# Kernel optimization log

Measured on AMD Instinct MI355X. Metric: run time of the kernel, lower is better.

Reference implementation:

```python
import jax, jax.numpy as jnp
import numpy as np

N_NODES = 100000
N_EDGES = 300000
NUM_GRAPHS = 2000
IN_DIM = 82
HIDDEN = 256


def _gcn_conv(x, src, dst, dinv, W, b):
    # GCNConv: out = D^-1/2 (A + I) D^-1/2 (x W) + b
    xW = x @ W  # [N, H]
    norm = dinv[src] * dinv[dst]  # [E]
    agg = jax.ops.segment_sum(xW[src] * norm[:, None], dst, num_segments=N_NODES)
    self_loop = xW * (dinv * dinv)[:, None]
    return agg + self_loop + b


def setup_inputs() -> dict:
    key = jax.random.key(0)
    ks = jax.random.split(key, 8)
    x = jax.random.normal(ks[0], (N_NODES, IN_DIM), dtype=jnp.float32)
    edge_index = jax.random.randint(ks[1], (2, N_EDGES), 0, N_NODES, dtype=jnp.int64)
    batch = jnp.sort(jax.random.randint(ks[2], (N_NODES,), 0, NUM_GRAPHS, dtype=jnp.int64))
    W1 = jax.random.normal(ks[3], (IN_DIM, HIDDEN), dtype=jnp.float32) * (1.0 / np.sqrt(IN_DIM))
    W2 = jax.random.normal(ks[4], (HIDDEN, HIDDEN), dtype=jnp.float32) * (1.0 / np.sqrt(HIDDEN))
    W3 = jax.random.normal(ks[5], (HIDDEN, HIDDEN), dtype=jnp.float32) * (1.0 / np.sqrt(HIDDEN))
    b1 = jnp.zeros((HIDDEN,), jnp.float32)
    b2 = jnp.zeros((HIDDEN,), jnp.float32)
    b3 = jnp.zeros((HIDDEN,), jnp.float32)
    return {"x": x, "edge_index": edge_index, "batch": batch, "num_graphs": NUM_GRAPHS,
            "W1": W1, "b1": b1, "W2": W2, "b2": b2, "W3": W3, "b3": b3}


def reference(x, edge_index, batch, num_graphs, W1, b1, W2, b2, W3, b3):
    src, dst = edge_index[0], edge_index[1]
    # symmetric normalization with added self-loops (PyG gcn_norm)
    deg = jax.ops.segment_sum(jnp.ones_like(dst, dtype=x.dtype), dst, num_segments=N_NODES) + 1.0
    dinv = jax.lax.rsqrt(deg)
    h = jax.nn.relu(_gcn_conv(x, src, dst, dinv, W1, b1))
    h = jax.nn.relu(_gcn_conv(h, src, dst, dinv, W2, b2))
    h = jax.nn.relu(_gcn_conv(h, src, dst, dinv, W3, b3))
    return jax.ops.segment_max(h, batch, num_segments=num_graphs)  # [G, H]
```

## Files before the change

kernel.cpp:

```cpp
#include <hip/hip_runtime.h>
#include <cstdint>
#include <cstddef>

#define N_NODES 100000
#define N_EDGES 300000
#define N_GRAPHS 2000
#define HID 256
#define INDIM 82
#define XCPAD 84
#define K1PAD 128
#define N_TILES ((N_NODES + 255) / 256)
#define SCAN_CHUNK 2048
#define NBLK_SCAN ((N_NODES + SCAN_CHUNK - 1) / SCAN_CHUNK)

typedef __bf16 bf16x8 __attribute__((ext_vector_type(8)));
typedef float f32x4 __attribute__((ext_vector_type(4)));

__device__ __forceinline__ unsigned short f2bf(float f) {
    union { __bf16 h; unsigned short u; } v;
    v.h = (__bf16)f;
    return v.u;
}
__device__ __forceinline__ float bf2f(unsigned short s) {
    return __uint_as_float(((unsigned int)s) << 16);
}
__device__ __forceinline__ int sig(int c) { return ((c & 15) << 4) | (c >> 4); }

__global__ void k_cnt_acc(const int* __restrict__ ei, int* cnt) {
    int e = blockIdx.x * 256 + threadIdx.x;
    if (e < N_EDGES) atomicAdd(&cnt[ei[N_EDGES + e]], 1);
}

__global__ __launch_bounds__(256) void k_scan1(const int* __restrict__ cnt, int* __restrict__ off,
                                               int* __restrict__ partial) {
    __shared__ int sdata[256];
    const int base = blockIdx.x * SCAN_CHUNK;
    const int t = threadIdx.x;
    int v[8];
    int s = 0;
#pragma unroll
    for (int i = 0; i < 8; ++i) {
        int idx = base + t * 8 + i;
        v[i] = (idx < N_NODES) ? cnt[idx] : 0;
        s += v[i];
    }
    sdata[t] = s;
    __syncthreads();
    for (int d = 1; d < 256; d <<= 1) {
        int x = (t >= d) ? sdata[t - d] : 0;
        __syncthreads();
        sdata[t] += x;
        __syncthreads();
    }
    int run = sdata[t] - s;
#pragma unroll
    for (int i = 0; i < 8; ++i) {
        int idx = base + t * 8 + i;
        if (idx < N_NODES) off[idx] = run;
        run += v[i];
    }
    if (t == 255) partial[blockIdx.x] = sdata[255];
}

__global__ void k_scan2(int* partial) {
    if (threadIdx.x == 0 && blockIdx.x == 0) {
        int run = 0;
        for (int i = 0; i < NBLK_SCAN; ++i) {
            int v = partial[i];
            partial[i] = run;
            run += v;
        }
    }
}

__global__ void k_scan3(int* __restrict__ off, const int* __restrict__ partial,
                        int* __restrict__ cur, const int* __restrict__ cnt,
                        float* __restrict__ dinv) {
    int i = blockIdx.x * 256 + threadIdx.x;
    if (i < N_NODES) {
        int o = off[i] + partial[i >> 11];
        off[i] = o;
        cur[i] = o;
        dinv[i] = rsqrtf((float)cnt[i] + 1.0f);
    }
}

__global__ void k_fill(const int* __restrict__ ei, const float* __restrict__ dinv, int* cur,
                       int* __restrict__ csr_src, float* __restrict__ csr_norm) {
    int e = blockIdx.x * 256 + threadIdx.x;
    if (e < N_EDGES) {
        int s = ei[e];
        int d = ei[N_EDGES + e];
        int pos = atomicAdd(&cur[d], 1);
        csr_src[pos] = s;
        csr_norm[pos] = dinv[s] * dinv[d];
    }
}

__device__ __forceinline__ void wconv_body(const float* __restrict__ W,
                                           unsigned short* __restrict__ Wb, int KSRC, int i,
                                           bool perm) {
    int kc = i >> 13;
    int r = i & 8191;
    int nt = r >> 9;
    int r2 = r & 511;
    int lg = r2 >> 7;
    int lr = (r2 >> 3) & 15;
    int j = r2 & 7;
    int k = kc * 32 + lg * 8 + j;
    if (perm) k = sig(k);
    int n = nt * 16 + lr;
    Wb[i] = (k < KSRC) ? f2bf(W[(size_t)k * HID + n]) : (unsigned short)0;
}

#define PREP_W1 128
#define PREP_W23 256
#define PREP_BND 8
#define PREP_XC ((N_NODES * XCPAD + 255) / 256)
#define PREP_BLOCKS (PREP_W1 + 2 * PREP_W23 + PREP_BND + PREP_XC)

__global__ void k_prep(const float* __restrict__ x, unsigned short* __restrict__ xc,
                       const float* __restrict__ W1, unsigned short* __restrict__ Wb1,
                       const float* __restrict__ W2, unsigned short* __restrict__ Wb2,
                       const float* __restrict__ W3, unsigned short* __restrict__ Wb3,
                       const int* __restrict__ batch, int* __restrict__ gstart) {
    int b = blockIdx.x;
    int t = threadIdx.x;
    if (b < PREP_W1) { wconv_body(W1, Wb1, INDIM, b * 256 + t, false); return; }
    b -= PREP_W1;
    if (b < PREP_W23) { wconv_body(W2, Wb2, HID, b * 256 + t, true); return; }
    b -= PREP_W23;
    if (b < PREP_W23) { wconv_body(W3, Wb3, HID, b * 256 + t, true); return; }
    b -= PREP_W23;
    if (b < PREP_BND) {
        int g = b * 256 + t;
        if (g <= N_GRAPHS) {
            int lo = 0, hi = N_NODES;
            while (lo < hi) {
                int mid = (lo + hi) >> 1;
                if (batch[mid] < g) lo = mid + 1;
                else hi = mid;
            }
            gstart[g] = lo;
        }
        return;
    }
    b -= PREP_BND;
    int i = b * 256 + t;
    if (i < N_NODES * XCPAD) {
        int node = i / XCPAD;
        int k = i - node * XCPAD;
        xc[i] = (k < INDIM) ? f2bf(x[(size_t)node * INDIM + k]) : (unsigned short)0;
    }
}

template <int K>
__global__ __launch_bounds__(512) void k_gemm_mfma(const unsigned short* __restrict__ A,
                                                   const unsigned short* __restrict__ Wb,
                                                   const float* __restrict__ bias,
                                                   unsigned short* __restrict__ Cb) {
    constexpr int NK = K / 32;
    __shared__ __align__(16) unsigned short Wsh[K * HID];

    const int tid = threadIdx.x;
    const int w = tid >> 6;
    const int l = tid & 63;
    const int lr = l & 15;
    const int lg = l >> 4;

#pragma unroll
    for (int i = 0; i < K / 16; ++i) {
        int o = (i * 512 + tid) * 8;
        *reinterpret_cast<uint4*>(&Wsh[o]) = *reinterpret_cast<const uint4*>(Wb + o);
    }
    __syncthreads();

    float bv[16];
#pragma unroll
    for (int nt = 0; nt < 16; ++nt) bv[nt] = bias[nt * 16 + lr];

    for (int t = blockIdx.x; t < N_TILES; t += 256) {
        const int rowbase = t * 256 + w * 32;
        int r0 = rowbase + lr;
        int r1 = rowbase + 16 + lr;
        int r0c = r0 < N_NODES ? r0 : (N_NODES - 1);
        int r1c = r1 < N_NODES ? r1 : (N_NODES - 1);
        const unsigned short* a0p = A + (size_t)r0c * K + lg * 8;
        const unsigned short* a1p = A + (size_t)r1c * K + lg * 8;

        bf16x8 a0[NK], a1[NK];
#pragma unroll
        for (int kc = 0; kc < NK; ++kc) {
            a0[kc] = *reinterpret_cast<const bf16x8*>(a0p + kc * 32);
            a1[kc] = *reinterpret_cast<const bf16x8*>(a1p + kc * 32);
        }

        f32x4 acc0[16] = {};
        f32x4 acc1[16] = {};

#pragma unroll
        for (int kc = 0; kc < NK; ++kc) {
            const unsigned short* bfp = Wsh + kc * 8192 + l * 8;
#pragma unroll
            for (int nt = 0; nt < 16; ++nt) {
                bf16x8 bb = *reinterpret_cast<const bf16x8*>(bfp + nt * 512);
                acc0[nt] = __builtin_amdgcn_mfma_f32_16x16x32_bf16(a0[kc], bb, acc0[nt], 0, 0, 0);
                acc1[nt] = __builtin_amdgcn_mfma_f32_16x16x32_bf16(a1[kc], bb, acc1[nt], 0, 0, 0);
            }
        }

        int gr0 = rowbase + lg * 4;
#pragma unroll
        for (int j = 0; j < 4; ++j) {
            int gr = gr0 + j;
            if (gr < N_NODES) {
                unsigned short t0[16];
#pragma unroll
                for (int nt = 0; nt < 16; ++nt)
                    t0[nt] = f2bf(fmaxf(acc0[nt][j] + bv[nt], 0.0f));
                unsigned short* p = Cb + (size_t)gr * HID + lr * 16;
                *reinterpret_cast<uint4*>(p) = *reinterpret_cast<const uint4*>(t0);
                *reinterpret_cast<uint4*>(p + 8) = *reinterpret_cast<const uint4*>(t0 + 8);
            }
            int gr2 = gr + 16;
            if (gr2 < N_NODES) {
                unsigned short t1[16];
#pragma unroll
                for (int nt = 0; nt < 16; ++nt)
                    t1[nt] = f2bf(fmaxf(acc1[nt][j] + bv[nt], 0.0f));
                unsigned short* p = Cb + (size_t)gr2 * HID + lr * 16;
                *reinterpret_cast<uint4*>(p) = *reinterpret_cast<const uint4*>(t1);
                *reinterpret_cast<uint4*>(p + 8) = *reinterpret_cast<const uint4*>(t1 + 8);
            }
        }
    }
}

__global__ void k_aggregate256(const unsigned short* __restrict__ tb,
                               const float* __restrict__ dinv, const int* __restrict__ off,
                               const int* __restrict__ cnt, const int* __restrict__ csr_src,
                               const float* __restrict__ csr_norm,
                               unsigned short* __restrict__ ob) {
    int node = blockIdx.x * 4 + (threadIdx.x >> 6);
    if (node >= N_NODES) return;
    int lane = threadIdx.x & 63;
    const size_t lo = (size_t)lane * 4;
    int o0 = off[node];
    int n = cnt[node];
    float di = dinv[node];
    float s2 = di * di;
    ushort4 sv = *reinterpret_cast<const ushort4*>(&tb[(size_t)node * HID + lo]);
    float4 acc = {bf2f(sv.x) * s2, bf2f(sv.y) * s2, bf2f(sv.z) * s2, bf2f(sv.w) * s2};

    int j = 0;
    for (; j + 3 < n; j += 4) {
        int s0 = csr_src[o0 + j];
        int s1 = csr_src[o0 + j + 1];
        int s2i = csr_src[o0 + j + 2];
        int s3 = csr_src[o0 + j + 3];
        float n0 = csr_norm[o0 + j];
        float n1 = csr_norm[o0 + j + 1];
        float n2 = csr_norm[o0 + j + 2];
        float n3 = csr_norm[o0 + j + 3];
        ushort4 u0 = *reinterpret_cast<const ushort4*>(&tb[(size_t)s0 * HID + lo]);
        ushort4 u1 = *reinterpret_cast<const ushort4*>(&tb[(size_t)s1 * HID + lo]);
        ushort4 u2 = *reinterpret_cast<const ushort4*>(&tb[(size_t)s2i * HID + lo]);
        ushort4 u3 = *reinterpret_cast<const ushort4*>(&tb[(size_t)s3 * HID + lo]);
        acc.x = fmaf(n0, bf2f(u0.x), acc.x); acc.y = fmaf(n0, bf2f(u0.y), acc.y);
        acc.z = fmaf(n0, bf2f(u0.z), acc.z); acc.w = fmaf(n0, bf2f(u0.w), acc.w);
        acc.x = fmaf(n1, bf2f(u1.x), acc.x); acc.y = fmaf(n1, bf2f(u1.y), acc.y);
        acc.z = fmaf(n1, bf2f(u1.z), acc.z); acc.w = fmaf(n1, bf2f(u1.w), acc.w);
        acc.x = fmaf(n2, bf2f(u2.x), acc.x); acc.y = fmaf(n2, bf2f(u2.y), acc.y);
        acc.z = fmaf(n2, bf2f(u2.z), acc.z); acc.w = fmaf(n2, bf2f(u2.w), acc.w);
        acc.x = fmaf(n3, bf2f(u3.x), acc.x); acc.y = fmaf(n3, bf2f(u3.y), acc.y);
        acc.z = fmaf(n3, bf2f(u3.z), acc.z); acc.w = fmaf(n3, bf2f(u3.w), acc.w);
    }
    int rem = n - j;
    if (rem & 2) {
        int s0 = csr_src[o0 + j];
        int s1 = csr_src[o0 + j + 1];
        float n0 = csr_norm[o0 + j];
        float n1 = csr_norm[o0 + j + 1];
        ushort4 u0 = *reinterpret_cast<const ushort4*>(&tb[(size_t)s0 * HID + lo]);
        ushort4 u1 = *reinterpret_cast<const ushort4*>(&tb[(size_t)s1 * HID + lo]);
        acc.x = fmaf(n0, bf2f(u0.x), acc.x); acc.y = fmaf(n0, bf2f(u0.y), acc.y);
        acc.z = fmaf(n0, bf2f(u0.z), acc.z); acc.w = fmaf(n0, bf2f(u0.w), acc.w);
        acc.x = fmaf(n1, bf2f(u1.x), acc.x); acc.y = fmaf(n1, bf2f(u1.y), acc.y);
        acc.z = fmaf(n1, bf2f(u1.z), acc.z); acc.w = fmaf(n1, bf2f(u1.w), acc.w);
        j += 2;
    }
    if (rem & 1) {
        int s0 = csr_src[o0 + j];
        float n0 = csr_norm[o0 + j];
        ushort4 u0 = *reinterpret_cast<const ushort4*>(&tb[(size_t)s0 * HID + lo]);
        acc.x = fmaf(n0, bf2f(u0.x), acc.x); acc.y = fmaf(n0, bf2f(u0.y), acc.y);
        acc.z = fmaf(n0, bf2f(u0.z), acc.z); acc.w = fmaf(n0, bf2f(u0.w), acc.w);
    }
    ushort4 o;
    o.x = f2bf(acc.x);
    o.y = f2bf(acc.y);
    o.z = f2bf(acc.z);
    o.w = f2bf(acc.w);
    *reinterpret_cast<ushort4*>(&ob[(size_t)node * HID + lo]) = o;
}

__global__ void k_aggx(const unsigned short* __restrict__ xc,
                       const float* __restrict__ dinv, const int* __restrict__ off,
                       const int* __restrict__ cnt, const int* __restrict__ csr_src,
                       const float* __restrict__ csr_norm,
                       unsigned short* __restrict__ ob) {
    int node = blockIdx.x * 4 + (threadIdx.x >> 6);
    if (node >= N_NODES) return;
    int lane = threadIdx.x & 63;
    const bool act = lane < (XCPAD / 2);
    const size_t co = (size_t)lane * 2;
    int o0 = off[node];
    int n = cnt[node];
    float di = dinv[node];
    float s2 = di * di;
    float2 acc = {0.0f, 0.0f};
    if (act) {
        ushort2 sv = *reinterpret_cast<const ushort2*>(&xc[(size_t)node * XCPAD + co]);
        acc.x = bf2f(sv.x) * s2;
        acc.y = bf2f(sv.y) * s2;
    }
    int j = 0;
    for (; j + 3 < n; j += 4) {
        int s0 = csr_src[o0 + j];
        int s1 = csr_src[o0 + j + 1];
        int s2i = csr_src[o0 + j + 2];
        int s3 = csr_src[o0 + j + 3];
        float n0 = csr_norm[o0 + j];
        float n1 = csr_norm[o0 + j + 1];
        float n2 = csr_norm[o0 + j + 2];
        float n3 = csr_norm[o0 + j + 3];
        if (act) {
            ushort2 u0 = *reinterpret_cast<const ushort2*>(&xc[(size_t)s0 * XCPAD + co]);
            ushort2 u1 = *reinterpret_cast<const ushort2*>(&xc[(size_t)s1 * XCPAD + co]);
            ushort2 u2 = *reinterpret_cast<const ushort2*>(&xc[(size_t)s2i * XCPAD + co]);
            ushort2 u3 = *reinterpret_cast<const ushort2*>(&xc[(size_t)s3 * XCPAD + co]);
            acc.x = fmaf(n0, bf2f(u0.x), acc.x); acc.y = fmaf(n0, bf2f(u0.y), acc.y);
            acc.x = fmaf(n1, bf2f(u1.x), acc.x); acc.y = fmaf(n1, bf2f(u1.y), acc.y);
            acc.x = fmaf(n2, bf2f(u2.x), acc.x); acc.y = fmaf(n2, bf2f(u2.y), acc.y);
            acc.x = fmaf(n3, bf2f(u3.x), acc.x); acc.y = fmaf(n3, bf2f(u3.y), acc.y);
        }
    }
    int rem = n - j;
    if (rem & 2) {
        int s0 = csr_src[o0 + j];
        int s1 = csr_src[o0 + j + 1];
        float n0 = csr_norm[o0 + j];
        float n1 = csr_norm[o0 + j + 1];
        if (act) {
            ushort2 u0 = *reinterpret_cast<const ushort2*>(&xc[(size_t)s0 * XCPAD + co]);
            ushort2 u1 = *reinterpret_cast<const ushort2*>(&xc[(size_t)s1 * XCPAD + co]);
            acc.x = fmaf(n0, bf2f(u0.x), acc.x); acc.y = fmaf(n0, bf2f(u0.y), acc.y);
            acc.x = fmaf(n1, bf2f(u1.x), acc.x); acc.y = fmaf(n1, bf2f(u1.y), acc.y);
        }
        j += 2;
    }
    if (rem & 1) {
        int s0 = csr_src[o0 + j];
        float n0 = csr_norm[o0 + j];
        if (act) {
            ushort2 u0 = *reinterpret_cast<const ushort2*>(&xc[(size_t)s0 * XCPAD + co]);
            acc.x = fmaf(n0, bf2f(u0.x), acc.x); acc.y = fmaf(n0, bf2f(u0.y), acc.y);
        }
    }
    ushort2 o;
    o.x = f2bf(acc.x);
    o.y = f2bf(acc.y);
    *reinterpret_cast<ushort2*>(&ob[(size_t)node * K1PAD + co]) = o;
}

__global__ void k_pool2(const unsigned short* __restrict__ hb, const int* __restrict__ gstart,
                        float* __restrict__ out) {
    int g = blockIdx.x;
    int w = threadIdx.x >> 6;
    int lane = threadIdx.x & 63;
    int p = w * 128 + lane * 2;
    int s = gstart[g], e = gstart[g + 1];
    float2 m = {0.0f, 0.0f};
    for (int i = s; i < e; ++i) {
        ushort2 u = *reinterpret_cast<const ushort2*>(&hb[(size_t)i * HID + p]);
        m.x = fmaxf(m.x, bf2f(u.x));
        m.y = fmaxf(m.y, bf2f(u.y));
    }
    out[(size_t)g * HID + sig(p)] = m.x;
    out[(size_t)g * HID + sig(p + 1)] = m.y;
}

extern "C" void kernel_launch(void* const* d_in, const int* in_sizes, int n_in,
                              void* d_out, int out_size, void* d_ws, size_t ws_size,
                              hipStream_t stream) {
    const float* x = (const float*)d_in[0];
    const int* ei = (const int*)d_in[1];
    const int* batch = (const int*)d_in[2];
    const float* W1 = (const float*)d_in[4];
    const float* b1 = (const float*)d_in[5];
    const float* W2 = (const float*)d_in[6];
    const float* b2 = (const float*)d_in[7];
    const float* W3 = (const float*)d_in[8];
    const float* b3 = (const float*)d_in[9];
    float* out = (float*)d_out;

    char* ws = (char*)d_ws;
    float* dinv = (float*)(ws);
    int* cnt = (int*)(ws + (512 << 10));
    int* off = (int*)(ws + (1024 << 10));
    int* cur = (int*)(ws + (1536 << 10));
    int* part = (int*)(ws + (2048 << 10));
    int* gstart = (int*)(ws + (2048 << 10) + 4096);
    int* csr_src = (int*)(ws + (2176 << 10));
    float* csr_norm = (float*)(ws + (3392 << 10));
    unsigned short* Wb1 = (unsigned short*)(ws + (4608 << 10));
    unsigned short* Wb2 = (unsigned short*)(ws + (4736 << 10));
    unsigned short* Wb3 = (unsigned short*)(ws + (4928 << 10));
    unsigned short* ag1_b = (unsigned short*)(ws + (5120 << 10));
    unsigned short* bufA = (unsigned short*)(ws + (5120 << 10) + 25600000);
    unsigned short* bufB = (unsigned short*)(ws + (5120 << 10) + 76800000);
    unsigned short* x_c = (unsigned short*)(ws + (5120 << 10) + 128000000);

    const int nblk_edges = (N_EDGES + 255) / 256;
    const int nblk_nodes = (N_NODES + 255) / 256;
    const int nblk_rows4 = (N_NODES + 3) / 4;

    hipMemsetAsync(cnt, 0, N_NODES * sizeof(int), stream);
    k_cnt_acc<<<nblk_edges, 256, 0, stream>>>(ei, cnt);
    k_scan1<<<NBLK_SCAN, 256, 0, stream>>>(cnt, off, part);
    k_scan2<<<1, 64, 0, stream>>>(part);
    k_scan3<<<nblk_nodes, 256, 0, stream>>>(off, part, cur, cnt, dinv);
    k_fill<<<nblk_edges, 256, 0, stream>>>(ei, dinv, cur, csr_src, csr_norm);

    k_prep<<<PREP_BLOCKS, 256, 0, stream>>>(x, x_c, W1, Wb1, W2, Wb2, W3, Wb3, batch, gstart);

    k_aggx<<<nblk_rows4, 256, 0, stream>>>(x_c, dinv, off, cnt, csr_src, csr_norm, ag1_b);
    k_gemm_mfma<K1PAD><<<256, 512, 0, stream>>>(ag1_b, Wb1, b1, bufA);

    k_aggregate256<<<nblk_rows4, 256, 0, stream>>>(bufA, dinv, off, cnt, csr_src, csr_norm, bufB);
    k_gemm_mfma<HID><<<256, 512, 0, stream>>>(bufB, Wb2, b2, bufA);

    k_aggregate256<<<nblk_rows4, 256, 0, stream>>>(bufA, dinv, off, cnt, csr_src, csr_norm, bufB);
    k_gemm_mfma<HID><<<256, 512, 0, stream>>>(bufB, Wb3, b3, bufA);

    k_pool2<<<N_GRAPHS, 128, 0, stream>>>(bufA, gstart, out);
}
```

Before: 254.8 us.

## Split GEMM output columns across two blocks per tile to raise occupancy

The MFMA GEMM kernel now gives each block one row tile and half of the 256 output columns, where before a persistent loop over tiles covered all columns. The shared weight copy is halved and the accumulator and A-register arrays shrink, with launch bounds requesting 4 blocks per SM. Grid size grows from 256 persistent blocks to about 784, and tile indexing pairs neighbouring half-blocks so they share A rows in cache. The cost is that each A row is loaded twice and the weight-to-shared staging is repeated per block instead of being amortized across tiles.

```diff
diff --git a/kernel.cpp b/kernel.cpp
--- a/kernel.cpp
+++ b/kernel.cpp
@@ -10,6 +10,7 @@
 #define XCPAD 84
 #define K1PAD 128
 #define N_TILES ((N_NODES + 255) / 256)
+#define GEMM_GRID (((N_TILES + 7) / 8) * 16)
 #define SCAN_CHUNK 2048
 #define NBLK_SCAN ((N_NODES + SCAN_CHUNK - 1) / SCAN_CHUNK)
 
@@ -155,12 +156,17 @@
 }
 
 template <int K>
-__global__ __launch_bounds__(512) void k_gemm_mfma(const unsigned short* __restrict__ A,
-                                                   const unsigned short* __restrict__ Wb,
-                                                   const float* __restrict__ bias,
-                                                   unsigned short* __restrict__ Cb) {
+__global__ __launch_bounds__(512, 4) void k_gemm_mfma(const unsigned short* __restrict__ A,
+                                                      const unsigned short* __restrict__ Wb,
+                                                      const float* __restrict__ bias,
+                                                      unsigned short* __restrict__ Cb) {
     constexpr int NK = K / 32;
-    __shared__ __align__(16) unsigned short Wsh[K * HID];
+    __shared__ __align__(16) unsigned short Wsh[K * 128];
+
+    const int b = blockIdx.x;
+    const int h = (b >> 3) & 1;
+    const int t = (b & 7) | ((b >> 4) << 3);
+    if (t >= N_TILES) return;
 
     const int tid = threadIdx.x;
     const int w = tid >> 6;
@@ -169,69 +175,60 @@
     const int lg = l >> 4;
 
 #pragma unroll
-    for (int i = 0; i < K / 16; ++i) {
-        int o = (i * 512 + tid) * 8;
-        *reinterpret_cast<uint4*>(&Wsh[o]) = *reinterpret_cast<const uint4*>(Wb + o);
+    for (int i = 0; i < NK; ++i) {
+        *reinterpret_cast<uint4*>(&Wsh[i * 4096 + tid * 8]) =
+            *reinterpret_cast<const uint4*>(Wb + i * 8192 + h * 4096 + tid * 8);
     }
     __syncthreads();
 
-    float bv[16];
-#pragma unroll
-    for (int nt = 0; nt < 16; ++nt) bv[nt] = bias[nt * 16 + lr];
-
-    for (int t = blockIdx.x; t < N_TILES; t += 256) {
-        const int rowbase = t * 256 + w * 32;
-        int r0 = rowbase + lr;
-        int r1 = rowbase + 16 + lr;
-        int r0c = r0 < N_NODES ? r0 : (N_NODES - 1);
-        int r1c = r1 < N_NODES ? r1 : (N_NODES - 1);
-        const unsigned short* a0p = A + (size_t)r0c * K + lg * 8;
-        const unsigned short* a1p = A + (size_t)r1c * K + lg * 8;
-
-        bf16x8 a0[NK], a1[NK];
-#pragma unroll
-        for (int kc = 0; kc < NK; ++kc) {
-            a0[kc] = *reinterpret_cast<const bf16x8*>(a0p + kc * 32);
-            a1[kc] = *reinterpret_cast<const bf16x8*>(a1p + kc * 32);
-        }
-
-        f32x4 acc0[16] = {};
-        f32x4 acc1[16] = {};
-
-#pragma unroll
-        for (int kc = 0; kc < NK; ++kc) {
-            const unsigned short* bfp = Wsh + kc * 8192 + l * 8;
-#pragma unroll
-            for (int nt = 0; nt < 16; ++nt) {
-                bf16x8 bb = *reinterpret_cast<const bf16x8*>(bfp + nt * 512);
-                acc0[nt] = __builtin_amdgcn_mfma_f32_16x16x32_bf16(a0[kc], bb, acc0[nt], 0, 0, 0);
-                acc1[nt] = __builtin_amdgcn_mfma_f32_16x16x32_bf16(a1[kc], bb, acc1[nt], 0, 0, 0);
-            }
-        }
-
-        int gr0 = rowbase + lg * 4;
-#pragma unroll
-        for (int j = 0; j < 4; ++j) {
-            int gr = gr0 + j;
-            if (gr < N_NODES) {
-                unsigned short t0[16];
-#pragma unroll
-                for (int nt = 0; nt < 16; ++nt)
-                    t0[nt] = f2bf(fmaxf(acc0[nt][j] + bv[nt], 0.0f));
-                unsigned short* p = Cb + (size_t)gr * HID + lr * 16;
-                *reinterpret_cast<uint4*>(p) = *reinterpret_cast<const uint4*>(t0);
-                *reinterpret_cast<uint4*>(p + 8) = *reinterpret_cast<const uint4*>(t0 + 8);
-            }
-            int gr2 = gr + 16;
-            if (gr2 < N_NODES) {
-                unsigned short t1[16];
-#pragma unroll
-                for (int nt = 0; nt < 16; ++nt)
-                    t1[nt] = f2bf(fmaxf(acc1[nt][j] + bv[nt], 0.0f));
-                unsigned short* p = Cb + (size_t)gr2 * HID + lr * 16;
-                *reinterpret_cast<uint4*>(p) = *reinterpret_cast<const uint4*>(t1);
-                *reinterpret_cast<uint4*>(p + 8) = *reinterpret_cast<const uint4*>(t1 + 8);
-            }
+    float bv[8];
+#pragma unroll
+    for (int nt = 0; nt < 8; ++nt) bv[nt] = bias[h * 128 + nt * 16 + lr];
+
+    const int rowbase = t * 256 + w * 32;
+    int r0 = rowbase + lr;
+    int r1 = rowbase + 16 + lr;
+    int r0c = r0 < N_NODES ? r0 : (N_NODES - 1);
+    int r1c = r1 < N_NODES ? r1 : (N_NODES - 1);
+    const unsigned short* a0p = A + (size_t)r0c * K + lg * 8;
+    const unsigned short* a1p = A + (size_t)r1c * K + lg * 8;
+
+    f32x4 acc0[8] = {};
+    f32x4 acc1[8] = {};
+
+#pragma unroll
+    for (int kc = 0; kc < NK; ++kc) {
+        bf16x8 a0 = *reinterpret_cast<const bf16x8*>(a0p + kc * 32);
+        bf16x8 a1 = *reinterpret_cast<const bf16x8*>(a1p + kc * 32);
+        const unsigned short* bfp = Wsh + kc * 4096 + l * 8;
+#pragma unroll
+        for (int nt = 0; nt < 8; ++nt) {
+            bf16x8 bb = *reinterpret_cast<const bf16x8*>(bfp + nt * 512);
+            acc0[nt] = __builtin_amdgcn_mfma_f32_16x16x32_bf16(a0, bb, acc0[nt], 0, 0, 0);
+            acc1[nt] = __builtin_amdgcn_mfma_f32_16x16x32_bf16(a1, bb, acc1[nt], 0, 0, 0);
+        }
+    }
+
+    int gr0 = rowbase + lg * 4;
+#pragma unroll
+    for (int j = 0; j < 4; ++j) {
+        int gr = gr0 + j;
+        if (gr < N_NODES) {
+            unsigned short t0[8];
+#pragma unroll
+            for (int nt = 0; nt < 8; ++nt)
+                t0[nt] = f2bf(fmaxf(acc0[nt][j] + bv[nt], 0.0f));
+            *reinterpret_cast<uint4*>(Cb + (size_t)gr * HID + lr * 16 + h * 8) =
+                *reinterpret_cast<const uint4*>(t0);
+        }
+        int gr2 = gr + 16;
+        if (gr2 < N_NODES) {
+            unsigned short t1[8];
+#pragma unroll
+            for (int nt = 0; nt < 8; ++nt)
+                t1[nt] = f2bf(fmaxf(acc1[nt][j] + bv[nt], 0.0f));
+            *reinterpret_cast<uint4*>(Cb + (size_t)gr2 * HID + lr * 16 + h * 8) =
+                *reinterpret_cast<const uint4*>(t1);
         }
     }
 }
@@ -435,13 +432,13 @@
     k_prep<<<PREP_BLOCKS, 256, 0, stream>>>(x, x_c, W1, Wb1, W2, Wb2, W3, Wb3, batch, gstart);
 
     k_aggx<<<nblk_rows4, 256, 0, stream>>>(x_c, dinv, off, cnt, csr_src, csr_norm, ag1_b);
-    k_gemm_mfma<K1PAD><<<256, 512, 0, stream>>>(ag1_b, Wb1, b1, bufA);
+    k_gemm_mfma<K1PAD><<<GEMM_GRID, 512, 0, stream>>>(ag1_b, Wb1, b1, bufA);
 
     k_aggregate256<<<nblk_rows4, 256, 0, stream>>>(bufA, dinv, off, cnt, csr_src, csr_norm, bufB);
-    k_gemm_mfma<HID><<<256, 512, 0, stream>>>(bufB, Wb2, b2, bufA);
+    k_gemm_mfma<HID><<<GEMM_GRID, 512, 0, stream>>>(bufB, Wb2, b2, bufA);
 
     k_aggregate256<<<nblk_rows4, 256, 0, stream>>>(bufA, dinv, off, cnt, csr_src, csr_norm, bufB);
-    k_gemm_mfma<HID><<<256, 512, 0, stream>>>(bufB, Wb3, b3, bufA);
+    k_gemm_mfma<HID><<<GEMM_GRID, 512, 0, stream>>>(bufB, Wb3, b3, bufA);
 
     k_pool2<<<N_GRAPHS, 128, 0, stream>>>(bufA, gstart, out);
 }
```

Result: slower. 268.7 us (+5.4%).
